# Optimization experiments

Hardware: AMD Instinct MI355X
Metric: run time of the kernel (lower is better)

The kernel has to match this reference:

```python
import jax, jax.numpy as jnp
import numpy as np

T, IN, H, OUT = 4096, 1024, 1024, 512


def setup_inputs() -> dict:
    key = jax.random.key(0)
    ks = jax.random.split(key, 7)
    s_g = 1.0 / np.sqrt(H + IN)  # xavier-ish scale for gate weights
    s_y = 1.0 / np.sqrt(H)
    return {
        "x": jax.random.normal(ks[0], (T, IN), jnp.float32),
        "wf": jax.random.normal(ks[1], (H, H + IN), jnp.float32) * s_g,
        "bf": jnp.zeros((H,), jnp.float32),
        "wi": jax.random.normal(ks[2], (H, H + IN), jnp.float32) * s_g,
        "bi": jnp.zeros((H,), jnp.float32),
        "wc": jax.random.normal(ks[3], (H, H + IN), jnp.float32) * s_g,
        "bc": jnp.zeros((H,), jnp.float32),
        "wo": jax.random.normal(ks[4], (H, H + IN), jnp.float32) * s_g,
        "bo": jnp.zeros((H,), jnp.float32),
        "why": jax.random.normal(ks[5], (OUT, H), jnp.float32) * s_y,
        "by": jnp.zeros((OUT,), jnp.float32),
    }


def reference(x, wf, bf, wi, bi, wc, bc, wo, bo, why, by):
    hid = wf.shape[0]

    def step(carry, x_t):
        h, c = carry
        concat = jnp.concatenate([h, x_t])  # (H+IN,)
        f = jax.nn.sigmoid(wf @ concat + bf)
        i = jax.nn.sigmoid(wi @ concat + bi)
        o = jax.nn.sigmoid(wo @ concat + bo)
        g = jnp.tanh(wc @ concat + bc)
        c_new = f * c + i * g
        h_new = o * jnp.tanh(c_new)
        y = why @ h_new + by  # (OUT,)
        return (h_new, c_new), y

    h0 = jnp.zeros((hid,), x.dtype)
    c0 = jnp.zeros((hid,), x.dtype)
    (h, c), ys = jax.lax.scan(step, (h0, c0), x)
    return ys, h, c
```

## Files before the change

### kernel.cpp

```cpp
#include <hip/hip_runtime.h>
#include <stdint.h>

#define TT 4096
#define INW 1024
#define HW 1024
#define OUTW 512
#define CH 2048


__device__ __forceinline__ uint64_t pack_pair(float v, uint32_t ep) {
    return ((uint64_t)ep << 32) | (uint64_t)__float_as_uint(v);
}
__device__ __forceinline__ float sigmoid_fast(float z) {
    return 1.0f / (1.0f + __expf(-z));
}
__device__ __forceinline__ float tanh_fast(float z) {
    return 1.0f - 2.0f / (1.0f + __expf(2.0f * z));
}

template <int CTRL>
__device__ __forceinline__ float dpp_add(float v) {
    int s = __builtin_amdgcn_update_dpp(0, __float_as_int(v), CTRL, 0xF, 0xF, true);
    return v + __int_as_float(s);
}
__device__ __forceinline__ float wave_sum_to_lane63(float v) {
    v = dpp_add<0x111>(v);
    v = dpp_add<0x112>(v);
    v = dpp_add<0x114>(v);
    v = dpp_add<0x118>(v);
    v = dpp_add<0x142>(v);
    v = dpp_add<0x143>(v);
    return v;
}

__global__ void lstm_init_kernel(uint64_t* __restrict__ hpair) {
    int j = blockIdx.x * blockDim.x + threadIdx.x;
    if (j < HW) {
        hpair[j]      = pack_pair(0.0f, 0u);
        hpair[HW + j] = pack_pair(0.0f, 0x80000000u);
    }
}

__global__ __launch_bounds__(256, 1) void lstm_seq_kernel(
    const float* __restrict__ x,
    const float* __restrict__ wf, const float* __restrict__ bf,
    const float* __restrict__ wi, const float* __restrict__ bi,
    const float* __restrict__ wc, const float* __restrict__ bc,
    const float* __restrict__ wo, const float* __restrict__ bo,
    uint64_t* __restrict__ hpair, float* __restrict__ h_all,
    float* __restrict__ out)
{
    __shared__ float hsh[2][HW];

    const int tid  = threadIdx.x;
    const int lane = tid & 63;
    const int w    = tid >> 6;
    const int b    = blockIdx.x;
    const int gu   = b * 4 + w;

    int kmap[16];
#pragma unroll
    for (int s = 0; s < 4; ++s) kmap[s] = 4 * w + s;
#pragma unroll
    for (int s = 4; s < 16; ++s) kmap[s] = 4 * ((w + 1 + ((s - 4) >> 2)) & 3) + (s & 3);

    float wh[64], wx[64];
    {
        const float* wptr[4] = {wf, wi, wc, wo};
#pragma unroll
        for (int g = 0; g < 4; ++g) {
            const float* base = wptr[g] + (size_t)gu * CH + lane;
#pragma unroll
            for (int s = 0; s < 16; ++s) wh[g * 16 + s] = base[(size_t)kmap[s] * 64];
#pragma unroll
            for (int k = 0; k < 16; ++k) wx[g * 16 + k] = base[1024 + (size_t)k * 64];
        }
    }
#pragma unroll
    for (int i = 0; i < 64; ++i) {
        asm volatile("" : "+v"(wh[i]));
        asm volatile("" : "+v"(wx[i]));
    }

    const float bias0 = bf[gu];
    const float bias1 = bi[gu];
    const float bias2 = bc[gu];
    const float bias3 = bo[gu];

    float xacc0 = (lane == 63) ? bias0 : 0.f;
    float xacc1 = (lane == 63) ? bias1 : 0.f;
    float xacc2 = (lane == 63) ? bias2 : 0.f;
    float xacc3 = (lane == 63) ? bias3 : 0.f;
    {
        const float* xp = x + lane;
        float xv[16];
#pragma unroll
        for (int k = 0; k < 16; ++k) xv[k] = xp[(size_t)k * 64];
#pragma unroll
        for (int k = 0; k < 16; ++k) {
            xacc0 = fmaf(wx[0 * 16 + k], xv[k], xacc0);
            xacc1 = fmaf(wx[1 * 16 + k], xv[k], xacc1);
            xacc2 = fmaf(wx[2 * 16 + k], xv[k], xacc2);
            xacc3 = fmaf(wx[3 * 16 + k], xv[k], xacc3);
        }
    }

    float c = 0.0f, h_last = 0.0f;

    for (int t = 0; t < TT; ++t) {
        const int p = t & 1;

        const uint64_t* hp = hpair + (size_t)p * HW + 256 * w + lane;
        float hq[4];
        {
            bool ok;
            do {
                uint64_t pv[4];
#pragma unroll
                for (int k = 0; k < 4; ++k)
                    pv[k] = __hip_atomic_load(&hp[64 * k],
                                              __ATOMIC_RELAXED, __HIP_MEMORY_SCOPE_SYSTEM);
                ok = true;
#pragma unroll
                for (int k = 0; k < 4; ++k)
                    ok &= ((uint32_t)(pv[k] >> 32) == (uint32_t)t);
#pragma unroll
                for (int k = 0; k < 4; ++k)
                    hq[k] = __uint_as_float((uint32_t)pv[k]);
            } while (!__all(ok));
        }

#pragma unroll
        for (int k = 0; k < 4; ++k)
            hsh[p][256 * w + lane + 64 * k] = hq[k];

        float acc0 = xacc0, acc1 = xacc1, acc2 = xacc2, acc3 = xacc3;
#pragma unroll
        for (int j = 0; j < 4; ++j) {
            acc0 = fmaf(wh[0 * 16 + j], hq[j], acc0);
            acc1 = fmaf(wh[1 * 16 + j], hq[j], acc1);
            acc2 = fmaf(wh[2 * 16 + j], hq[j], acc2);
            acc3 = fmaf(wh[3 * 16 + j], hq[j], acc3);
        }
        __syncthreads();

        float xn[16];
        {
            const int tn = (t + 1 < TT) ? t + 1 : t;
            const float* xp = x + (size_t)tn * INW + lane;
#pragma unroll
            for (int k = 0; k < 16; ++k) xn[k] = xp[(size_t)k * 64];
        }

        if (t >= 1 && b == (t & 255)) {
            float4 hv4 = *(const float4*)&hsh[p][tid * 4];
            *(float4*)(h_all + (size_t)(t - 1) * HW + tid * 4) = hv4;
        }

#pragma unroll
        for (int i = 0; i < 3; ++i) {
            const int q = (w + 1 + i) & 3;
            const float* hrow = &hsh[p][256 * q + lane];
#pragma unroll
            for (int j = 0; j < 4; ++j) {
                const float v = hrow[64 * j];
                const int s = 4 + i * 4 + j;
                acc0 = fmaf(wh[0 * 16 + s], v, acc0);
                acc1 = fmaf(wh[1 * 16 + s], v, acc1);
                acc2 = fmaf(wh[2 * 16 + s], v, acc2);
                acc3 = fmaf(wh[3 * 16 + s], v, acc3);
            }
        }

        acc0 = wave_sum_to_lane63(acc0);
        acc1 = wave_sum_to_lane63(acc1);
        acc2 = wave_sum_to_lane63(acc2);
        acc3 = wave_sum_to_lane63(acc3);

        if (lane == 63) {
            float f  = sigmoid_fast(acc0);
            float ii = sigmoid_fast(acc1);
            float g  = tanh_fast(acc2);
            float o  = sigmoid_fast(acc3);
            c = fmaf(f, c, ii * g);
            float hn = o * tanh_fast(c);
            h_last = hn;
            __hip_atomic_store(&hpair[(size_t)((t + 1) & 1) * HW + gu],
                               pack_pair(hn, (uint32_t)(t + 1)),
                               __ATOMIC_RELAXED, __HIP_MEMORY_SCOPE_SYSTEM);
        }
        __builtin_amdgcn_sched_barrier(0);

        float nx0 = (lane == 63) ? bias0 : 0.f;
        float nx1 = (lane == 63) ? bias1 : 0.f;
        float nx2 = (lane == 63) ? bias2 : 0.f;
        float nx3 = (lane == 63) ? bias3 : 0.f;
#pragma unroll
        for (int k = 0; k < 16; ++k) {
            nx0 = fmaf(wx[0 * 16 + k], xn[k], nx0);
            nx1 = fmaf(wx[1 * 16 + k], xn[k], nx1);
            nx2 = fmaf(wx[2 * 16 + k], xn[k], nx2);
            nx3 = fmaf(wx[3 * 16 + k], xn[k], nx3);
        }
        xacc0 = nx0; xacc1 = nx1; xacc2 = nx2; xacc3 = nx3;
    }

    if (lane == 63) {
        h_all[(size_t)(TT - 1) * HW + gu] = h_last;
        out[(size_t)TT * OUTW + gu]      = h_last;
        out[(size_t)TT * OUTW + HW + gu] = c;
    }
}

__global__ __launch_bounds__(256) void lstm_ygemm_kernel(
    const float* __restrict__ hall, const float* __restrict__ why,
    const float* __restrict__ by, float* __restrict__ ys)
{
    __shared__ float hs[64][17];
    __shared__ float wsm[64][17];
    const int t0 = blockIdx.x * 64, o0 = blockIdx.y * 64;
    const int tid = threadIdx.x;
    const int tx = tid & 15, ty = tid >> 4;

    float acc[4][4] = {};
    const int r = tid >> 2;
    const int cc = (tid & 3) * 4;

    for (int kk = 0; kk < HW; kk += 16) {
        float4 hv = *(const float4*)(hall + (size_t)(t0 + r) * HW + kk + cc);
        hs[r][cc + 0] = hv.x; hs[r][cc + 1] = hv.y;
        hs[r][cc + 2] = hv.z; hs[r][cc + 3] = hv.w;
        float4 wv = *(const float4*)(why + (size_t)(o0 + r) * HW + kk + cc);
        wsm[r][cc + 0] = wv.x; wsm[r][cc + 1] = wv.y;
        wsm[r][cc + 2] = wv.z; wsm[r][cc + 3] = wv.w;
        __syncthreads();
#pragma unroll
        for (int k = 0; k < 16; ++k) {
            float ha[4], wa[4];
#pragma unroll
            for (int i = 0; i < 4; ++i) ha[i] = hs[ty * 4 + i][k];
#pragma unroll
            for (int j = 0; j < 4; ++j) wa[j] = wsm[tx * 4 + j][k];
#pragma unroll
            for (int i = 0; i < 4; ++i)
#pragma unroll
                for (int j = 0; j < 4; ++j)
                    acc[i][j] = fmaf(ha[i], wa[j], acc[i][j]);
        }
        __syncthreads();
    }
#pragma unroll
    for (int i = 0; i < 4; ++i) {
#pragma unroll
        for (int j = 0; j < 4; ++j) {
            int oo = o0 + tx * 4 + j;
            ys[(size_t)(t0 + ty * 4 + i) * OUTW + oo] = acc[i][j] + by[oo];
        }
    }
}

extern "C" void kernel_launch(void* const* d_in, const int* in_sizes, int n_in,
                              void* d_out, int out_size, void* d_ws, size_t ws_size,
                              hipStream_t stream) {
    const float* x   = (const float*)d_in[0];
    const float* wf  = (const float*)d_in[1];
    const float* bf  = (const float*)d_in[2];
    const float* wi  = (const float*)d_in[3];
    const float* bi  = (const float*)d_in[4];
    const float* wc  = (const float*)d_in[5];
    const float* bc  = (const float*)d_in[6];
    const float* wo  = (const float*)d_in[7];
    const float* bo  = (const float*)d_in[8];
    const float* why = (const float*)d_in[9];
    const float* by  = (const float*)d_in[10];
    float* out = (float*)d_out;

    uint64_t* hpair = (uint64_t*)d_ws;
    float* h_all = (float*)((char*)d_ws + (size_t)2 * HW * sizeof(uint64_t));

    lstm_init_kernel<<<dim3(4), dim3(256), 0, stream>>>(hpair);
    lstm_seq_kernel<<<dim3(256), dim3(256), 0, stream>>>(
        x, wf, bf, wi, bi, wc, bc, wo, bo, hpair, h_all, out);
    lstm_ygemm_kernel<<<dim3(64, 8), dim3(256), 0, stream>>>(h_all, why, by, out);
}
```

Before: 6.773 ms.

## Fuse output projection into persistent LSTM recurrence kernel

Drops the separate y-GEMM kernel and the h_all history buffer. In each step, two waves per block compute one output row of why·h from the shared-memory copy of the previous h and write it directly to the output. A final spin-wait after the loop collects the last hidden state for the last output row. This removes one kernel launch and a 16 MB write and read of the hidden history. The cost is extra per-step work and 16 more weight registers in the latency-bound critical loop.

```diff
diff --git a/kernel.cpp b/kernel.cpp
--- a/kernel.cpp
+++ b/kernel.cpp
@@ -47,8 +47,8 @@
     const float* __restrict__ wi, const float* __restrict__ bi,
     const float* __restrict__ wc, const float* __restrict__ bc,
     const float* __restrict__ wo, const float* __restrict__ bo,
-    uint64_t* __restrict__ hpair, float* __restrict__ h_all,
-    float* __restrict__ out)
+    const float* __restrict__ why, const float* __restrict__ by,
+    uint64_t* __restrict__ hpair, float* __restrict__ out)
 {
     __shared__ float hsh[2][HW];
 
@@ -81,6 +81,22 @@
         asm volatile("" : "+v"(wh[i]));
         asm volatile("" : "+v"(wx[i]));
     }
+
+    const int yo = 2 * b + w;
+    float wy[16];
+    float ybias = 0.f;
+    if (w < 2) {
+        const float* yb = why + (size_t)yo * HW + lane;
+#pragma unroll
+        for (int k = 0; k < 16; ++k) wy[k] = yb[(size_t)k * 64];
+        ybias = by[yo];
+    } else {
+#pragma unroll
+        for (int k = 0; k < 16; ++k) wy[k] = 0.f;
+    }
+#pragma unroll
+    for (int i = 0; i < 16; ++i)
+        asm volatile("" : "+v"(wy[i]));
 
     const float bias0 = bf[gu];
     const float bias1 = bi[gu];
@@ -150,11 +166,6 @@
             const float* xp = x + (size_t)tn * INW + lane;
 #pragma unroll
             for (int k = 0; k < 16; ++k) xn[k] = xp[(size_t)k * 64];
-        }
-
-        if (t >= 1 && b == (t & 255)) {
-            float4 hv4 = *(const float4*)&hsh[p][tid * 4];
-            *(float4*)(h_all + (size_t)(t - 1) * HW + tid * 4) = hv4;
         }
 
 #pragma unroll
@@ -191,6 +202,16 @@
         }
         __builtin_amdgcn_sched_barrier(0);
 
+        if (w < 2 && t >= 1) {
+            float yacc = (lane == 63) ? ybias : 0.f;
+#pragma unroll
+            for (int k = 0; k < 16; ++k)
+                yacc = fmaf(wy[k], hsh[p][lane + 64 * k], yacc);
+            yacc = wave_sum_to_lane63(yacc);
+            if (lane == 63)
+                out[(size_t)(t - 1) * OUTW + yo] = yacc;
+        }
+
         float nx0 = (lane == 63) ? bias0 : 0.f;
         float nx1 = (lane == 63) ? bias1 : 0.f;
         float nx2 = (lane == 63) ? bias2 : 0.f;
@@ -205,57 +226,43 @@
         xacc0 = nx0; xacc1 = nx1; xacc2 = nx2; xacc3 = nx3;
     }
 
+    {
+        const int p = TT & 1;
+        const uint64_t* hp = hpair + (size_t)p * HW + 256 * w + lane;
+        float hq[4];
+        bool ok;
+        do {
+            uint64_t pv[4];
+#pragma unroll
+            for (int k = 0; k < 4; ++k)
+                pv[k] = __hip_atomic_load(&hp[64 * k],
+                                          __ATOMIC_RELAXED, __HIP_MEMORY_SCOPE_SYSTEM);
+            ok = true;
+#pragma unroll
+            for (int k = 0; k < 4; ++k)
+                ok &= ((uint32_t)(pv[k] >> 32) == (uint32_t)TT);
+#pragma unroll
+            for (int k = 0; k < 4; ++k)
+                hq[k] = __uint_as_float((uint32_t)pv[k]);
+        } while (!__all(ok));
+#pragma unroll
+        for (int k = 0; k < 4; ++k)
+            hsh[p][256 * w + lane + 64 * k] = hq[k];
+        __syncthreads();
+        if (w < 2) {
+            float yacc = (lane == 63) ? ybias : 0.f;
+#pragma unroll
+            for (int k = 0; k < 16; ++k)
+                yacc = fmaf(wy[k], hsh[p][lane + 64 * k], yacc);
+            yacc = wave_sum_to_lane63(yacc);
+            if (lane == 63)
+                out[(size_t)(TT - 1) * OUTW + yo] = yacc;
+        }
+    }
+
     if (lane == 63) {
-        h_all[(size_t)(TT - 1) * HW + gu] = h_last;
         out[(size_t)TT * OUTW + gu]      = h_last;
         out[(size_t)TT * OUTW + HW + gu] = c;
-    }
-}
-
-__global__ __launch_bounds__(256) void lstm_ygemm_kernel(
-    const float* __restrict__ hall, const float* __restrict__ why,
-    const float* __restrict__ by, float* __restrict__ ys)
-{
-    __shared__ float hs[64][17];
-    __shared__ float wsm[64][17];
-    const int t0 = blockIdx.x * 64, o0 = blockIdx.y * 64;
-    const int tid = threadIdx.x;
-    const int tx = tid & 15, ty = tid >> 4;
-
-    float acc[4][4] = {};
-    const int r = tid >> 2;
-    const int cc = (tid & 3) * 4;
-
-    for (int kk = 0; kk < HW; kk += 16) {
-        float4 hv = *(const float4*)(hall + (size_t)(t0 + r) * HW + kk + cc);
-        hs[r][cc + 0] = hv.x; hs[r][cc + 1] = hv.y;
-        hs[r][cc + 2] = hv.z; hs[r][cc + 3] = hv.w;
-        float4 wv = *(const float4*)(why + (size_t)(o0 + r) * HW + kk + cc);
-        wsm[r][cc + 0] = wv.x; wsm[r][cc + 1] = wv.y;
-        wsm[r][cc + 2] = wv.z; wsm[r][cc + 3] = wv.w;
-        __syncthreads();
-#pragma unroll
-        for (int k = 0; k < 16; ++k) {
-            float ha[4], wa[4];
-#pragma unroll
-            for (int i = 0; i < 4; ++i) ha[i] = hs[ty * 4 + i][k];
-#pragma unroll
-            for (int j = 0; j < 4; ++j) wa[j] = wsm[tx * 4 + j][k];
-#pragma unroll
-            for (int i = 0; i < 4; ++i)
-#pragma unroll
-                for (int j = 0; j < 4; ++j)
-                    acc[i][j] = fmaf(ha[i], wa[j], acc[i][j]);
-        }
-        __syncthreads();
-    }
-#pragma unroll
-    for (int i = 0; i < 4; ++i) {
-#pragma unroll
-        for (int j = 0; j < 4; ++j) {
-            int oo = o0 + tx * 4 + j;
-            ys[(size_t)(t0 + ty * 4 + i) * OUTW + oo] = acc[i][j] + by[oo];
-        }
     }
 }
 
@@ -276,10 +283,8 @@
     float* out = (float*)d_out;
 
     uint64_t* hpair = (uint64_t*)d_ws;
-    float* h_all = (float*)((char*)d_ws + (size_t)2 * HW * sizeof(uint64_t));
 
     lstm_init_kernel<<<dim3(4), dim3(256), 0, stream>>>(hpair);
     lstm_seq_kernel<<<dim3(256), dim3(256), 0, stream>>>(
-        x, wf, bf, wi, bi, wc, bc, wo, bo, hpair, h_all, out);
-    lstm_ygemm_kernel<<<dim3(64, 8), dim3(256), 0, stream>>>(h_all, why, by, out);
-}
+        x, wf, bf, wi, bi, wc, bc, wo, bo, why, by, hpair, out);
+}
```

Measured after the change: 6.586 ms. -2.8%, faster.
